# Kernel optimization log

Hardware: AMD Instinct MI355X
Metric: run time of the kernel (lower is better)

The kernel has to match this reference:

```python
import jax, jax.numpy as jnp
import numpy as np

B, T_DEC, T_ENC = 64, 128, 256
D_IN, D_ENC, H = 256, 512, 512


def setup_inputs() -> dict:
    key = jax.random.key(0)
    ks = jax.random.split(key, 8)
    s = 0.05  # keras 'uniform' init is small; keep params modest
    return {
        "inputs": jax.random.normal(ks[0], (B, T_DEC, D_IN), jnp.float32),
        "context_mat": jax.random.normal(ks[1], (B, T_ENC, D_ENC), jnp.float32),
        "att_w1": jax.random.uniform(ks[2], (H + D_ENC, D_ENC), jnp.float32, -s, s),
        "att_w2": jax.random.uniform(ks[3], (D_ENC, 1), jnp.float32, -s, s),
        "Wx": jax.random.uniform(ks[4], (D_IN + D_ENC, 3 * H), jnp.float32, -s, s),
        "Wh": jax.random.uniform(ks[5], (H, 3 * H), jnp.float32, -s, s),
        "b": jnp.zeros((3 * H,), jnp.float32),
    }


def reference(inputs, context_mat, att_w1, att_w2, Wx, Wh, b):
    # inputs: [B, T_dec, d_in]; context_mat: [B, T_enc, d_enc]
    Bn, Te, De = context_mat.shape
    Hn = Wh.shape[0]

    def step(h, x_t):
        # --- Bahdanau-style attention (concat -> relu(MLP) -> softmax) ---
        key_rep = jnp.broadcast_to(h[:, None, :], (Bn, Te, Hn))
        concated = jnp.concatenate([key_rep, context_mat], axis=-1)  # [B,Te,H+De]
        energies = jax.nn.relu(
            jnp.einsum('bte,eo->bto', concated @ att_w1, att_w2)[..., 0]
        )  # [B, Te]
        att = jax.nn.softmax(energies, axis=-1)
        ctx = jnp.einsum('bt,btd->bd', att, context_mat)  # [B, De]
        # --- GRU cell (reset_after=False, classic Keras) ---
        xin = jnp.concatenate([x_t, ctx], axis=-1)  # [B, d_in+De]
        gx = xin @ Wx + b  # [B, 3H]
        xz, xr, xh = gx[:, :Hn], gx, gx  # slices below
        xz = gx[:, :Hn]
        xr = gx[:, Hn:2 * Hn]
        xh = gx[:, 2 * Hn:]
        z = jax.nn.sigmoid(xz + h @ Wh[:, :Hn])
        r = jax.nn.sigmoid(xr + h @ Wh[:, Hn:2 * Hn])
        hh = jnp.tanh(xh + (r * h) @ Wh[:, 2 * Hn:])
        h_new = z * h + (1.0 - z) * hh
        return h_new, h_new

    h0 = jnp.zeros((Bn, Hn), inputs.dtype)
    xs = jnp.swapaxes(inputs, 0, 1)  # [T_dec, B, d_in]
    _, outs = jax.lax.scan(step, h0, xs)  # [T_dec, B, H]
    return jnp.swapaxes(outs, 0, 1)  # [B, T_dec, H]
```

## Files before the change

kernel.cpp:

```cpp
#include <hip/hip_runtime.h>

#define NBLK  256
#define NTHR  384
#define TDEC  128
#define TENC  256
#define DIN   256
#define DENC  512
#define HHH   512
#define NG    1536
#define KTOT  1280
#define NK4   320
#define NCOL  384

#define OFF_CNT   0
#define OFF_HDOT  24576
#define OFF_U     57344
#define OFF_ECTX  58368
#define OFF_HG    74752
#define OFF_CTXG  107520
#define OFF_RHG   140288
#define OFF_WP    173056
#define WP_ELEMS  (4*NK4*NCOL*4)

__device__ __forceinline__ float wave_sum(float v) {
#pragma unroll
    for (int o = 32; o; o >>= 1) v += __shfl_down(v, o, 64);
    return v;
}
__device__ __forceinline__ float wave_max(float v) {
#pragma unroll
    for (int o = 32; o; o >>= 1) v = fmaxf(v, __shfl_down(v, o, 64));
    return v;
}
__device__ __forceinline__ float ldA(float* p) {
    return __hip_atomic_load(p, __ATOMIC_RELAXED, __HIP_MEMORY_SCOPE_AGENT);
}
__device__ __forceinline__ void stA(float* p, float v) {
    __hip_atomic_store(p, v, __ATOMIC_RELAXED, __HIP_MEMORY_SCOPE_AGENT);
}
__device__ __forceinline__ void drain_stores() {
    asm volatile("s_waitcnt vmcnt(0)" ::: "memory");
}
__device__ __forceinline__ void arrive(unsigned* c) {
    asm volatile("s_waitcnt vmcnt(0)" ::: "memory");
    __hip_atomic_fetch_add(c, 1u, __ATOMIC_RELAXED, __HIP_MEMORY_SCOPE_AGENT);
}
__device__ __forceinline__ void wait4(unsigned* c) {
    while (__hip_atomic_load(c, __ATOMIC_RELAXED, __HIP_MEMORY_SCOPE_AGENT) < 4u)
        __builtin_amdgcn_s_sleep(2);
}
__device__ __forceinline__ float blo(unsigned u) { return __uint_as_float(u << 16); }
__device__ __forceinline__ float bhi(unsigned u) { return __uint_as_float(u & 0xffff0000u); }
__device__ __forceinline__ unsigned short f2bf(float f) {
    unsigned u = __float_as_uint(f);
    u += 0x7fffu + ((u >> 16) & 1u);
    return (unsigned short)(u >> 16);
}

template<bool BF>
__device__ __forceinline__ float dotrange(const void* wp, size_t base, int c,
                                          int k4lo, int k4hi, const float4* a4,
                                          int aoff, float acc) {
    if (BF) {
        const uint2* w = (const uint2*)wp + base + c;
#pragma unroll 8
        for (int k4 = k4lo; k4 < k4hi; ++k4) {
            uint2 uu = w[(size_t)k4 * NCOL];
            float4 a = a4[k4 - aoff];
            acc = fmaf(blo(uu.x), a.x, acc);
            acc = fmaf(bhi(uu.x), a.y, acc);
            acc = fmaf(blo(uu.y), a.z, acc);
            acc = fmaf(bhi(uu.y), a.w, acc);
        }
    } else {
        const float4* w = (const float4*)wp + base + c;
#pragma unroll 8
        for (int k4 = k4lo; k4 < k4hi; ++k4) {
            float4 wv = w[(size_t)k4 * NCOL];
            float4 a = a4[k4 - aoff];
            acc = fmaf(wv.x, a.x, acc);
            acc = fmaf(wv.y, a.y, acc);
            acc = fmaf(wv.z, a.z, acc);
            acc = fmaf(wv.w, a.w, acc);
        }
    }
    return acc;
}

__global__ void k_u(const float* __restrict__ w1, const float* __restrict__ w2,
                    float* __restrict__ u) {
    int e = blockIdx.x;
    int lane = threadIdx.x;
    float p = 0.f;
#pragma unroll
    for (int k = lane; k < DENC; k += 64) p += w1[e*DENC + k] * w2[k];
    p = wave_sum(p);
    if (lane == 0) u[e] = p;
}

__global__ void k_ectx(const float* __restrict__ C, const float* __restrict__ u,
                       float* __restrict__ ectx) {
    int r = blockIdx.x*4 + (threadIdx.x >> 6);
    int lane = threadIdx.x & 63;
    const float* row = C + (size_t)r*DENC;
    const float* vc  = u + HHH;
    float p = 0.f;
#pragma unroll
    for (int k = 0; k < DENC/64; ++k) p += row[lane + k*64] * vc[lane + k*64];
    p = wave_sum(p);
    if (lane == 0) ectx[r] = p;
}

template<bool BF>
__global__ void k_wpack(const float* __restrict__ Wx, const float* __restrict__ Wh,
                        void* __restrict__ wp) {
    int id = blockIdx.x*256 + threadIdx.x;
    int e = id & 3;
    int q = id >> 2;
    int c = q % NCOL;
    q /= NCOL;
    int k4 = q % NK4;
    int js = q / NK4;
    int k = k4*4 + e;
    int col = (c >> 7)*512 + js*128 + (c & 127);
    float v = (k < 768) ? Wx[(size_t)k*NG + col] : Wh[(size_t)(k-768)*NG + col];
    if (BF) ((unsigned short*)wp)[id] = f2bf(v);
    else    ((float*)wp)[id] = v;
}

template<bool BF>
__launch_bounds__(NTHR, 1)
__global__ void decoder(const float* __restrict__ inp, const float* __restrict__ C,
                        const float* __restrict__ bias, const void* __restrict__ wpv,
                        const float* __restrict__ u, float* __restrict__ ectx_g,
                        float* __restrict__ out, float* __restrict__ ws) {
    unsigned* cnt = (unsigned*)ws;
    float* hdotP = ws + OFF_HDOT;
    float* hG    = ws + OFF_HG;
    float* ctxG  = ws + OFF_CTXG;
    float* rhG   = ws + OFF_RHG;

    const int tid = threadIdx.x;
    const int w   = tid >> 6;
    const int b   = blockIdx.x >> 2;
    const int js  = blockIdx.x & 3;
    const int c    = tid;
    const int gate = c >> 7;
    const int jp   = c & 127;

    __shared__ float sh_C[TENC*128];
    __shared__ __align__(16) float sh_kx[KTOT];
    __shared__ __align__(16) float sh_rh[HHH];
    __shared__ float sh_att[TENC];
    __shared__ float sh_ectx[TENC];
    __shared__ float sh_u[128];
    __shared__ float sh_z[128];
    __shared__ float sh_cred[2][128];
    __shared__ float sh_red[8];
    __shared__ float sh_scal;

    const float4* kx4 = (const float4*)sh_kx;
    const float4* rh4 = (const float4*)sh_rh;
    const size_t wbase = (size_t)js * NK4 * NCOL;

    for (int i = tid; i < TENC*128; i += NTHR) {
        int q = i >> 7, dp = i & 127;
        sh_C[i] = C[((size_t)b*TENC + q)*DENC + js*128 + dp];
    }
    if (tid < TENC) sh_ectx[tid] = ectx_g[b*TENC + tid];
    if (tid >= 256) sh_u[tid - 256] = u[js*128 + (tid - 256)];
    const float bias_c = bias[gate*512 + js*128 + jp];

    for (int t = 0; t < TDEC; ++t) {
        __syncthreads();
        if (tid < DIN) sh_kx[tid] = inp[((size_t)b*TDEC + t)*DIN + tid];
        __syncthreads();

        float acc = dotrange<BF>(wpv, wbase, c, 0, 64, kx4, 0, bias_c);

        if (t > 0) {
            if (tid == 0) {
                wait4(&cnt[((t-1)*3 + 2)*64 + b]);
                float s0 = ldA(&hdotP[(t-1)*256 + b*4 + 0]);
                float s1 = ldA(&hdotP[(t-1)*256 + b*4 + 1]);
                float s2 = ldA(&hdotP[(t-1)*256 + b*4 + 2]);
                float s3 = ldA(&hdotP[(t-1)*256 + b*4 + 3]);
                sh_scal = (s0 + s1) + (s2 + s3);
            }
            __syncthreads();
            for (int i = tid; i < HHH; i += NTHR) sh_kx[768 + i] = ldA(&hG[b*HHH + i]);
        } else {
            if (tid == 0) sh_scal = 0.f;
            for (int i = tid; i < HHH; i += NTHR) sh_kx[768 + i] = 0.f;
        }
        __syncthreads();
        const float hd = sh_scal;

        if (tid < TENC) {
            float e = fmaxf(hd + sh_ectx[tid], 0.f);
            float wm = wave_max(e);
            if ((tid & 63) == 0) sh_red[w] = wm;
            __syncthreads();
            float mx = fmaxf(fmaxf(sh_red[0], sh_red[1]), fmaxf(sh_red[2], sh_red[3]));
            float ex = __expf(e - mx);
            float wse = wave_sum(ex);
            __syncthreads();
            if ((tid & 63) == 0) sh_red[w] = wse;
            __syncthreads();
            float dn = sh_red[0] + sh_red[1] + sh_red[2] + sh_red[3];
            sh_att[tid] = ex / dn;
        } else {
            __syncthreads(); __syncthreads(); __syncthreads();
        }
        __syncthreads();

        if (tid < TENC) {
            const int dp = tid & 127, hf = tid >> 7;
            const float* Cl = sh_C + (size_t)hf*128*128 + dp;
            float a = 0.f;
#pragma unroll 8
            for (int q = 0; q < 128; ++q)
                a = fmaf(sh_att[hf*128 + q], Cl[(size_t)q*128], a);
            sh_cred[hf][dp] = a;
        }
        __syncthreads();
        if (tid < 128) stA(&ctxG[b*HHH + js*128 + tid], sh_cred[0][tid] + sh_cred[1][tid]);
        drain_stores();
        __syncthreads();
        if (tid == 0) arrive(&cnt[(t*3 + 0)*64 + b]);

        if (t > 0 && c < 256)
            acc = dotrange<BF>(wpv, wbase, c, 192, 320, kx4, 0, acc);

        if (tid == 0) wait4(&cnt[(t*3 + 0)*64 + b]);
        __syncthreads();
        for (int i = tid; i < HHH; i += NTHR) sh_kx[256 + i] = ldA(&ctxG[b*HHH + i]);
        __syncthreads();
        acc = dotrange<BF>(wpv, wbase, c, 64, 192, kx4, 0, acc);

        if (gate == 0) {
            sh_z[jp] = 1.f / (1.f + __expf(-acc));
        } else if (gate == 1) {
            float r = 1.f / (1.f + __expf(-acc));
            stA(&rhG[b*HHH + js*128 + jp], r * sh_kx[768 + js*128 + jp]);
        }
        drain_stores();
        __syncthreads();
        if (tid == 0) arrive(&cnt[(t*3 + 1)*64 + b]);

        if (tid == 0) wait4(&cnt[(t*3 + 1)*64 + b]);
        __syncthreads();
        for (int i = tid; i < HHH; i += NTHR) sh_rh[i] = ldA(&rhG[b*HHH + i]);
        __syncthreads();

        if (gate == 2) {
            acc = dotrange<BF>(wpv, wbase, c, 192, 320, rh4, 192, acc);
            float hh = tanhf(acc);
            float z  = sh_z[jp];
            float hp = sh_kx[768 + js*128 + jp];
            float hn = z*hp + (1.f - z)*hh;
            stA(&hG[b*HHH + js*128 + jp], hn);
            out[((size_t)b*TDEC + t)*HHH + js*128 + jp] = hn;
            float p = sh_u[jp] * hn;
            float s = wave_sum(p);
            if ((tid & 63) == 0) sh_red[w] = s;
        }
        drain_stores();
        __syncthreads();
        if (tid == 0) {
            stA(&hdotP[t*256 + b*4 + js], sh_red[4] + sh_red[5]);
            arrive(&cnt[(t*3 + 2)*64 + b]);
        }
    }
}

extern "C" void kernel_launch(void* const* d_in, const int* in_sizes, int n_in,
                              void* d_out, int out_size, void* d_ws, size_t ws_size,
                              hipStream_t stream) {
    const float* inputs = (const float*)d_in[0];
    const float* C      = (const float*)d_in[1];
    const float* w1     = (const float*)d_in[2];
    const float* w2     = (const float*)d_in[3];
    const float* Wx     = (const float*)d_in[4];
    const float* Wh     = (const float*)d_in[5];
    const float* bias   = (const float*)d_in[6];
    float* out = (float*)d_out;
    float* ws  = (float*)d_ws;

    hipMemsetAsync(ws, 0, 128*3*64*sizeof(unsigned), stream);

    k_u   <<<1024, 64,  0, stream>>>(w1, w2, ws + OFF_U);
    k_ectx<<<(64*TENC)/4, 256, 0, stream>>>(C, ws + OFF_U, ws + OFF_ECTX);

    const size_t need_f32 = (size_t)(OFF_WP) * 4u + (size_t)WP_ELEMS * 4u;
    void* wp = (void*)(ws + OFF_WP);
    if (ws_size >= need_f32) {
        k_wpack<false><<<WP_ELEMS/256, 256, 0, stream>>>(Wx, Wh, wp);
        decoder<false><<<NBLK, NTHR, 0, stream>>>(inputs, C, bias, wp,
                                                  ws + OFF_U, ws + OFF_ECTX, out, ws);
    } else {
        k_wpack<true><<<WP_ELEMS/256, 256, 0, stream>>>(Wx, Wh, wp);
        decoder<true><<<NBLK, NTHR, 0, stream>>>(inputs, C, bias, wp,
                                                 ws + OFF_U, ws + OFF_ECTX, out, ws);
    }
}
```

Baseline: 3.253 ms.

## Repartition GRU matmul across 4-batch groups to reuse weights across batches

Blocks now cover a group of 4 batch rows and a 32-column slice of each gate, not one batch row and 128 columns. Each weight load from the packed buffer is reused across 4 batch elements held interleaved in shared memory, which cuts weight traffic by a factor of four. The attention h·u dot is now computed locally from the gathered hidden state, replacing the cross-block partial-sum exchange. In exchange, each barrier waits on 16 blocks instead of 4, and every step gathers more state from global memory into shared memory.

```diff
diff --git a/kernel.cpp b/kernel.cpp
--- a/kernel.cpp
+++ b/kernel.cpp
@@ -10,17 +10,15 @@
 #define NG    1536
 #define KTOT  1280
 #define NK4   320
-#define NCOL  384
 
 #define OFF_CNT   0
-#define OFF_HDOT  24576
-#define OFF_U     57344
-#define OFF_ECTX  58368
-#define OFF_HG    74752
-#define OFF_CTXG  107520
-#define OFF_RHG   140288
-#define OFF_WP    173056
-#define WP_ELEMS  (4*NK4*NCOL*4)
+#define OFF_U     8192
+#define OFF_ECTX  9216
+#define OFF_HG    25600
+#define OFF_CTXG  58368
+#define OFF_RHG   91136
+#define OFF_WP    123904
+#define WP_ELEMS  (16*NK4*96*4)
 
 __device__ __forceinline__ float wave_sum(float v) {
 #pragma unroll
@@ -45,8 +43,8 @@
     asm volatile("s_waitcnt vmcnt(0)" ::: "memory");
     __hip_atomic_fetch_add(c, 1u, __ATOMIC_RELAXED, __HIP_MEMORY_SCOPE_AGENT);
 }
-__device__ __forceinline__ void wait4(unsigned* c) {
-    while (__hip_atomic_load(c, __ATOMIC_RELAXED, __HIP_MEMORY_SCOPE_AGENT) < 4u)
+__device__ __forceinline__ void wait16(unsigned* c) {
+    while (__hip_atomic_load(c, __ATOMIC_RELAXED, __HIP_MEMORY_SCOPE_AGENT) < 16u)
         __builtin_amdgcn_s_sleep(2);
 }
 __device__ __forceinline__ float blo(unsigned u) { return __uint_as_float(u << 16); }
@@ -58,26 +56,26 @@
 }
 
 template<bool BF>
-__device__ __forceinline__ float dotrange(const void* wp, size_t base, int c,
+__device__ __forceinline__ float dotrange(const void* wp, int cg, int col, int b,
                                           int k4lo, int k4hi, const float4* a4,
                                           int aoff, float acc) {
     if (BF) {
-        const uint2* w = (const uint2*)wp + base + c;
+        const uint2* w = (const uint2*)wp + (size_t)cg*NK4*96 + col;
 #pragma unroll 8
         for (int k4 = k4lo; k4 < k4hi; ++k4) {
-            uint2 uu = w[(size_t)k4 * NCOL];
-            float4 a = a4[k4 - aoff];
+            uint2 uu = w[(size_t)k4 * 96];
+            float4 a = a4[(k4 - aoff)*4 + b];
             acc = fmaf(blo(uu.x), a.x, acc);
             acc = fmaf(bhi(uu.x), a.y, acc);
             acc = fmaf(blo(uu.y), a.z, acc);
             acc = fmaf(bhi(uu.y), a.w, acc);
         }
     } else {
-        const float4* w = (const float4*)wp + base + c;
+        const float4* w = (const float4*)wp + (size_t)cg*NK4*96 + col;
 #pragma unroll 8
         for (int k4 = k4lo; k4 < k4hi; ++k4) {
-            float4 wv = w[(size_t)k4 * NCOL];
-            float4 a = a4[k4 - aoff];
+            float4 wv = w[(size_t)k4 * 96];
+            float4 a = a4[(k4 - aoff)*4 + b];
             acc = fmaf(wv.x, a.x, acc);
             acc = fmaf(wv.y, a.y, acc);
             acc = fmaf(wv.z, a.z, acc);
@@ -117,13 +115,13 @@
     int id = blockIdx.x*256 + threadIdx.x;
     int e = id & 3;
     int q = id >> 2;
-    int c = q % NCOL;
-    q /= NCOL;
+    int col = q % 96;
+    q /= 96;
     int k4 = q % NK4;
-    int js = q / NK4;
+    int cg = q / NK4;
     int k = k4*4 + e;
-    int col = (c >> 7)*512 + js*128 + (c & 127);
-    float v = (k < 768) ? Wx[(size_t)k*NG + col] : Wh[(size_t)(k-768)*NG + col];
+    int j = (col >> 5)*512 + cg*32 + (col & 31);
+    float v = (k < 768) ? Wx[(size_t)k*NG + j] : Wh[(size_t)(k-768)*NG + j];
     if (BF) ((unsigned short*)wp)[id] = f2bf(v);
     else    ((float*)wp)[id] = v;
 }
@@ -135,66 +133,77 @@
                         const float* __restrict__ u, float* __restrict__ ectx_g,
                         float* __restrict__ out, float* __restrict__ ws) {
     unsigned* cnt = (unsigned*)ws;
-    float* hdotP = ws + OFF_HDOT;
-    float* hG    = ws + OFF_HG;
-    float* ctxG  = ws + OFF_CTXG;
-    float* rhG   = ws + OFF_RHG;
-
-    const int tid = threadIdx.x;
-    const int w   = tid >> 6;
-    const int b   = blockIdx.x >> 2;
-    const int js  = blockIdx.x & 3;
-    const int c    = tid;
-    const int gate = c >> 7;
-    const int jp   = c & 127;
+    float* hG   = ws + OFF_HG;
+    float* ctxG = ws + OFF_CTXG;
+    float* rhG  = ws + OFF_RHG;
+
+    const int tid  = threadIdx.x;
+    const int w    = tid >> 6;
+    const int blk  = blockIdx.x;
+    const int bg   = blk >> 4;
+    const int cg   = blk & 15;
+    const int b_att = blk >> 2;
+    const int ds    = blk & 3;
+    const int bl_att = b_att & 3;
+    const int col  = tid >> 2;
+    const int b    = tid & 3;
+    const int sub  = col >> 5;
+    const int q32  = col & 31;
+    const int jp   = cg*32 + q32;
+    const int bglob = bg*4 + b;
 
     __shared__ float sh_C[TENC*128];
-    __shared__ __align__(16) float sh_kx[KTOT];
-    __shared__ __align__(16) float sh_rh[HHH];
+    __shared__ __align__(16) float sh_st[2048];
+    __shared__ __align__(16) float sh_h[2048];
     __shared__ float sh_att[TENC];
     __shared__ float sh_ectx[TENC];
-    __shared__ float sh_u[128];
+    __shared__ __align__(16) float sh_u[512];
     __shared__ float sh_z[128];
     __shared__ float sh_cred[2][128];
-    __shared__ float sh_red[8];
-    __shared__ float sh_scal;
-
-    const float4* kx4 = (const float4*)sh_kx;
-    const float4* rh4 = (const float4*)sh_rh;
-    const size_t wbase = (size_t)js * NK4 * NCOL;
-
-    for (int i = tid; i < TENC*128; i += NTHR) {
-        int q = i >> 7, dp = i & 127;
-        sh_C[i] = C[((size_t)b*TENC + q)*DENC + js*128 + dp];
-    }
-    if (tid < TENC) sh_ectx[tid] = ectx_g[b*TENC + tid];
-    if (tid >= 256) sh_u[tid - 256] = u[js*128 + (tid - 256)];
-    const float bias_c = bias[gate*512 + js*128 + jp];
+    __shared__ float sh_red[4];
+    __shared__ float sh_hdp[2];
+
+    const float4* st4 = (const float4*)sh_st;
+    const float4* h4f = (const float4*)sh_h;
+    const float4* u4  = (const float4*)sh_u;
+
+    for (int i = tid; i < TENC*128; i += NTHR)
+        sh_C[i] = C[((size_t)b_att*TENC + (i >> 7))*DENC + ds*128 + (i & 127)];
+    if (tid < TENC) sh_ectx[tid] = ectx_g[b_att*TENC + tid];
+    if (tid < 128) ((float4*)sh_u)[tid] = ((const float4*)(u))[tid];
+    const float bias_c = bias[sub*512 + jp];
 
     for (int t = 0; t < TDEC; ++t) {
         __syncthreads();
-        if (tid < DIN) sh_kx[tid] = inp[((size_t)b*TDEC + t)*DIN + tid];
-        __syncthreads();
-
-        float acc = dotrange<BF>(wpv, wbase, c, 0, 64, kx4, 0, bias_c);
+        for (int i = tid; i < 1024; i += NTHR) {
+            int bb = i >> 8, k = i & 255;
+            sh_st[((k >> 2)*4 + bb)*4 + (k & 3)] =
+                inp[((size_t)(bg*4 + bb)*TDEC + t)*DIN + k];
+        }
+        __syncthreads();
+
+        float acc = dotrange<BF>(wpv, cg, col, b, 0, 64, st4, 0, bias_c);
 
         if (t > 0) {
-            if (tid == 0) {
-                wait4(&cnt[((t-1)*3 + 2)*64 + b]);
-                float s0 = ldA(&hdotP[(t-1)*256 + b*4 + 0]);
-                float s1 = ldA(&hdotP[(t-1)*256 + b*4 + 1]);
-                float s2 = ldA(&hdotP[(t-1)*256 + b*4 + 2]);
-                float s3 = ldA(&hdotP[(t-1)*256 + b*4 + 3]);
-                sh_scal = (s0 + s1) + (s2 + s3);
-            }
+            if (tid == 0) wait16(cnt + (((t-1)*16 + bg) << 2) + 2);
             __syncthreads();
-            for (int i = tid; i < HHH; i += NTHR) sh_kx[768 + i] = ldA(&hG[b*HHH + i]);
-        } else {
-            if (tid == 0) sh_scal = 0.f;
-            for (int i = tid; i < HHH; i += NTHR) sh_kx[768 + i] = 0.f;
-        }
-        __syncthreads();
-        const float hd = sh_scal;
+        }
+        for (int i = tid; i < 2048; i += NTHR) {
+            int bb = i >> 9, j = i & 511;
+            sh_h[((j >> 2)*4 + bb)*4 + (j & 3)] =
+                (t > 0) ? ldA(&hG[(size_t)(bg*4 + bb)*HHH + j]) : 0.f;
+        }
+        __syncthreads();
+
+        if (tid < 128) {
+            float4 uu = u4[tid];
+            float4 hh = h4f[tid*4 + bl_att];
+            float p = uu.x*hh.x + uu.y*hh.y + uu.z*hh.z + uu.w*hh.w;
+            p = wave_sum(p);
+            if ((tid & 63) == 0) sh_hdp[w] = p;
+        }
+        __syncthreads();
+        const float hd = sh_hdp[0] + sh_hdp[1];
 
         if (tid < TENC) {
             float e = fmaxf(hd + sh_ectx[tid], 0.f);
@@ -224,53 +233,56 @@
             sh_cred[hf][dp] = a;
         }
         __syncthreads();
-        if (tid < 128) stA(&ctxG[b*HHH + js*128 + tid], sh_cred[0][tid] + sh_cred[1][tid]);
+        if (tid < 128) stA(&ctxG[(size_t)b_att*HHH + ds*128 + tid],
+                           sh_cred[0][tid] + sh_cred[1][tid]);
         drain_stores();
         __syncthreads();
-        if (tid == 0) arrive(&cnt[(t*3 + 0)*64 + b]);
-
-        if (t > 0 && c < 256)
-            acc = dotrange<BF>(wpv, wbase, c, 192, 320, kx4, 0, acc);
-
-        if (tid == 0) wait4(&cnt[(t*3 + 0)*64 + b]);
-        __syncthreads();
-        for (int i = tid; i < HHH; i += NTHR) sh_kx[256 + i] = ldA(&ctxG[b*HHH + i]);
-        __syncthreads();
-        acc = dotrange<BF>(wpv, wbase, c, 64, 192, kx4, 0, acc);
-
-        if (gate == 0) {
-            sh_z[jp] = 1.f / (1.f + __expf(-acc));
-        } else if (gate == 1) {
-            float r = 1.f / (1.f + __expf(-acc));
-            stA(&rhG[b*HHH + js*128 + jp], r * sh_kx[768 + js*128 + jp]);
+        if (tid == 0) arrive(cnt + ((t*16 + bg) << 2) + 0);
+
+        if (t > 0 && sub < 2)
+            acc = dotrange<BF>(wpv, cg, col, b, 192, 320, h4f, 192, acc);
+
+        if (tid == 0) wait16(cnt + ((t*16 + bg) << 2) + 0);
+        __syncthreads();
+        for (int i = tid; i < 2048; i += NTHR) {
+            int bb = i >> 9, j = i & 511;
+            sh_st[((j >> 2)*4 + bb)*4 + (j & 3)] =
+                ldA(&ctxG[(size_t)(bg*4 + bb)*HHH + j]);
+        }
+        __syncthreads();
+        acc = dotrange<BF>(wpv, cg, col, b, 64, 192, st4, 64, acc);
+
+        if (sub == 0) {
+            sh_z[q32*4 + b] = 1.f / (1.f + __expf(-acc));
+        } else if (sub == 1) {
+            float r  = 1.f / (1.f + __expf(-acc));
+            float hp = sh_h[((jp >> 2)*4 + b)*4 + (jp & 3)];
+            stA(&rhG[(size_t)bglob*HHH + jp], r * hp);
         }
         drain_stores();
         __syncthreads();
-        if (tid == 0) arrive(&cnt[(t*3 + 1)*64 + b]);
-
-        if (tid == 0) wait4(&cnt[(t*3 + 1)*64 + b]);
-        __syncthreads();
-        for (int i = tid; i < HHH; i += NTHR) sh_rh[i] = ldA(&rhG[b*HHH + i]);
-        __syncthreads();
-
-        if (gate == 2) {
-            acc = dotrange<BF>(wpv, wbase, c, 192, 320, rh4, 192, acc);
+        if (tid == 0) arrive(cnt + ((t*16 + bg) << 2) + 1);
+
+        if (tid == 0) wait16(cnt + ((t*16 + bg) << 2) + 1);
+        __syncthreads();
+        for (int i = tid; i < 2048; i += NTHR) {
+            int bb = i >> 9, j = i & 511;
+            sh_st[((j >> 2)*4 + bb)*4 + (j & 3)] =
+                ldA(&rhG[(size_t)(bg*4 + bb)*HHH + j]);
+        }
+        __syncthreads();
+        if (sub == 2) {
+            acc = dotrange<BF>(wpv, cg, col, b, 192, 320, st4, 192, acc);
             float hh = tanhf(acc);
-            float z  = sh_z[jp];
-            float hp = sh_kx[768 + js*128 + jp];
+            float z  = sh_z[q32*4 + b];
+            float hp = sh_h[((jp >> 2)*4 + b)*4 + (jp & 3)];
             float hn = z*hp + (1.f - z)*hh;
-            stA(&hG[b*HHH + js*128 + jp], hn);
-            out[((size_t)b*TDEC + t)*HHH + js*128 + jp] = hn;
-            float p = sh_u[jp] * hn;
-            float s = wave_sum(p);
-            if ((tid & 63) == 0) sh_red[w] = s;
+            stA(&hG[(size_t)bglob*HHH + jp], hn);
+            out[((size_t)bglob*TDEC + t)*HHH + jp] = hn;
         }
         drain_stores();
         __syncthreads();
-        if (tid == 0) {
-            stA(&hdotP[t*256 + b*4 + js], sh_red[4] + sh_red[5]);
-            arrive(&cnt[(t*3 + 2)*64 + b]);
-        }
+        if (tid == 0) arrive(cnt + ((t*16 + bg) << 2) + 2);
     }
 }
 
@@ -287,7 +299,7 @@
     float* out = (float*)d_out;
     float* ws  = (float*)d_ws;
 
-    hipMemsetAsync(ws, 0, 128*3*64*sizeof(unsigned), stream);
+    hipMemsetAsync(ws, 0, 128*16*4*sizeof(unsigned), stream);
 
     k_u   <<<1024, 64,  0, stream>>>(w1, w2, ws + OFF_U);
     k_ectx<<<(64*TENC)/4, 256, 0, stream>>>(C, ws + OFF_U, ws + OFF_ECTX);
```

After: 3.934 ms. +20.9%, slower.
